# Kernel tuning notes

Measured on AMD Instinct MI355X. Metric: run time of the kernel, lower is better.

Reference implementation:

```python
import jax, jax.numpy as jnp
import numpy as np

N_NODES = 100000
N_EDGES = 1600000
D_IN = 128
D_HID = 128
D_OUT = 1
N_GRAPHS = 64


def setup_inputs() -> dict:
    key = jax.random.key(0)
    ks = jax.random.split(key, 8)
    x = jax.random.normal(ks[0], (N_NODES, D_IN), dtype=jnp.float32)
    edge_index = jax.random.randint(ks[1], (2, N_EDGES), 0, N_NODES, dtype=jnp.int64)
    batch = jnp.sort(jax.random.randint(ks[2], (N_NODES,), 0, N_GRAPHS, dtype=jnp.int64))
    s1 = 1.0 / np.sqrt(D_IN)
    s2 = 1.0 / np.sqrt(D_HID)
    W1 = jax.random.normal(ks[3], (D_IN, D_HID), dtype=jnp.float32) * s1
    b1 = jnp.zeros((D_HID,), dtype=jnp.float32)
    W2 = jax.random.normal(ks[4], (D_HID, D_HID), dtype=jnp.float32) * s2
    b2 = jnp.zeros((D_HID,), dtype=jnp.float32)
    Wf = jax.random.normal(ks[5], (D_HID, D_OUT), dtype=jnp.float32) * s2
    bf = jnp.zeros((D_OUT,), dtype=jnp.float32)
    return {"x": x, "edge_index": edge_index, "batch": batch,
            "W1": W1, "b1": b1, "W2": W2, "b2": b2, "Wf": Wf, "bf": bf,
            "num_graphs": N_GRAPHS}


def reference(x, edge_index, batch, W1, b1, W2, b2, Wf, bf, num_graphs):
    n = x.shape[0]
    # GCNConv default: add self-loops, symmetric deg^{-1/2} normalization
    loop = jnp.arange(n, dtype=edge_index.dtype)
    src = jnp.concatenate([edge_index[0], loop])  # [E+N]
    dst = jnp.concatenate([edge_index[1], loop])
    deg = jax.ops.segment_sum(jnp.ones(src.shape, x.dtype), dst, num_segments=n)
    dinv = jnp.where(deg > 0, jax.lax.rsqrt(jnp.maximum(deg, 1.0)), 0.0)
    norm = dinv[src] * dinv[dst]  # [E+N]

    def gcn_conv(h, W, b):
        h = h @ W  # [N, d_out] linear first (GCNConv fuses lin before propagate)
        msg = h[src] * norm[:, None]  # gather + scale
        return jax.ops.segment_sum(msg, dst, num_segments=n) + b  # scatter-add

    h = jax.nn.relu(gcn_conv(x, W1, b1))
    h = jax.nn.relu(gcn_conv(h, W2, b2))

    # global_mean_pool over batch assignment
    gsum = jax.ops.segment_sum(h, batch, num_segments=num_graphs)
    cnt = jax.ops.segment_sum(jnp.ones((n,), x.dtype), batch, num_segments=num_graphs)
    pooled = gsum / jnp.maximum(cnt, 1.0)[:, None]  # [G, d_hid]

    return (pooled @ Wf + bf).squeeze(-1)  # [G]
```

## Files before the change

### kernel.cpp

```cpp
#include <hip/hip_runtime.h>
#include <hip/hip_bf16.h>
#include <math.h>


#define DFEAT 128
#define SCAN_NB 256
#define SCAN_TPB 256
#define FILL_CHUNKS 256

typedef unsigned int uint32;
typedef __attribute__((ext_vector_type(8))) short bf16x8;
typedef __attribute__((ext_vector_type(4))) float f32x4;

__device__ __forceinline__ uint32 f2bf_rne(float f) {
    uint32 x = __float_as_uint(f);
    return (x + 0x7fffu + ((x >> 16) & 1u)) >> 16;
}
__device__ __forceinline__ uint32 packbf2(float lo, float hi) {
    return f2bf_rne(lo) | (f2bf_rne(hi) << 16);
}

__global__ void k_zero2(int* __restrict__ a, int* __restrict__ b, int n) {
    int i = blockIdx.x * blockDim.x + threadIdx.x;
    if (i < n) { a[i] = 0; b[i] = 0; }
}

__global__ void k_zero_f(float* __restrict__ p, int n) {
    int i = blockIdx.x * blockDim.x + threadIdx.x;
    if (i < n) p[i] = 0.f;
}

__global__ void k_degcount(const int* __restrict__ dst, int* __restrict__ degcnt, int E) {
    int e = blockIdx.x * blockDim.x + threadIdx.x;
    if (e < E) atomicAdd(&degcnt[dst[e]], 1);
}

__global__ __launch_bounds__(256) void k_wt(const float* __restrict__ W,
                                            unsigned short* __restrict__ Wt) {
    int idx = blockIdx.x * 256 + threadIdx.x;
    if (idx < 128 * 128) {
        int n = idx >> 7, k = idx & 127;
        Wt[idx] = (unsigned short)f2bf_rne(W[(k << 7) + n]);
    }
}

__global__ __launch_bounds__(SCAN_TPB) void k_partsum(const int* __restrict__ deg,
                                                      int* __restrict__ bsum,
                                                      int N, int chunk) {
    int b = blockIdx.x, tid = threadIdx.x;
    int beg = b * chunk, end = min(N, beg + chunk);
    int s = 0;
    for (int i = beg + tid; i < end; i += SCAN_TPB) s += deg[i];
    __shared__ int lds[SCAN_TPB];
    lds[tid] = s;
    __syncthreads();
    for (int off = SCAN_TPB / 2; off > 0; off >>= 1) {
        if (tid < off) lds[tid] += lds[tid + off];
        __syncthreads();
    }
    if (tid == 0) bsum[b] = lds[0];
}

__global__ __launch_bounds__(SCAN_NB) void k_scanb(int* __restrict__ bsum) {
    __shared__ int lds[SCAN_NB];
    int tid = threadIdx.x;
    int v = bsum[tid];
    lds[tid] = v;
    __syncthreads();
    for (int off = 1; off < SCAN_NB; off <<= 1) {
        int t = (tid >= off) ? lds[tid - off] : 0;
        __syncthreads();
        lds[tid] += t;
        __syncthreads();
    }
    bsum[tid] = lds[tid] - v;
}

__global__ __launch_bounds__(SCAN_TPB) void k_writeptr(const int* __restrict__ deg,
                                                       const int* __restrict__ bbase,
                                                       int* __restrict__ rowptr,
                                                       float* __restrict__ dinv,
                                                       int N, int chunk) {
    int b = blockIdx.x, tid = threadIdx.x;
    int beg = b * chunk, end = min(N, beg + chunk);
    int per = (chunk + SCAN_TPB - 1) / SCAN_TPB;
    int tbeg = beg + tid * per;
    int tend = min(end, tbeg + per);
    int s = 0;
    for (int i = tbeg; i < tend; ++i) s += deg[i];
    __shared__ int lds[SCAN_TPB];
    lds[tid] = s;
    __syncthreads();
    for (int off = 1; off < SCAN_TPB; off <<= 1) {
        int t = (tid >= off) ? lds[tid - off] : 0;
        __syncthreads();
        lds[tid] += t;
        __syncthreads();
    }
    int run = bbase[b] + ((tid == 0) ? 0 : lds[tid - 1]);
    for (int i = tbeg; i < tend; ++i) {
        int d = deg[i];
        rowptr[i] = run;
        dinv[i] = rsqrtf((float)(d + 1));
        run += d;
    }
    if (tend == N && tbeg < tend) rowptr[N] = run;
}

__global__ __launch_bounds__(256) void k_fill(const int* __restrict__ src,
                                              const int* __restrict__ dst,
                                              const int* __restrict__ rowptr,
                                              int* __restrict__ fill,
                                              int* __restrict__ col, int E) {
    int r = blockIdx.x & 7;
    int chunk = blockIdx.x >> 3;
    int per = (E + FILL_CHUNKS - 1) / FILL_CHUNKS;
    int beg = chunk * per;
    int end = min(E, beg + per);
    for (int e = beg + threadIdx.x; e < end; e += 256) {
        int d = dst[e];
        if (((d >> 9) & 7) == r) {
            int pos = rowptr[d] + atomicAdd(&fill[d], 1);
            col[pos] = src[e];
        }
    }
}

__global__ __launch_bounds__(256, 3) void k_linear_mfma(const float* __restrict__ H,
                                                        const uint32* __restrict__ Wt,
                                                        uint32* __restrict__ C,
                                                        int N, int ntiles) {
    __shared__ uint32 WtS[128 * 64];
    __shared__ uint32 inS[64 * 64];
    int tid = threadIdx.x;
    int lane = tid & 63;
    int wv = tid >> 6;
    int g = lane >> 4;
    int r = lane & 15;
    int swz = (r & 7) << 4;
    {
        const uint4* srcp = (const uint4*)Wt;
#pragma unroll
        for (int i = 0; i < 8; ++i) {
            int c = tid + i * 256;
            int n = c >> 4, off = c & 15;
            int b = (n * 256 + off * 16) ^ ((n & 7) << 4);
            *(uint4*)((char*)WtS + b) = srcp[c];
        }
    }
    for (int t = blockIdx.x; t < ntiles; t += gridDim.x) {
        int rbase = t << 6;
        __syncthreads();
        {
            const float4* H4 = (const float4*)(H + (size_t)rbase * DFEAT);
            int limrow = N - rbase;
#pragma unroll
            for (int i = 0; i < 4; ++i) {
                int c = tid + i * 256;
                int m = c >> 4, off = c & 15;
                uint4 w2 = make_uint4(0u, 0u, 0u, 0u);
                if (m < limrow) {
                    float4 f0 = H4[m * 32 + off * 2];
                    float4 f1 = H4[m * 32 + off * 2 + 1];
                    w2.x = packbf2(f0.x, f0.y); w2.y = packbf2(f0.z, f0.w);
                    w2.z = packbf2(f1.x, f1.y); w2.w = packbf2(f1.z, f1.w);
                }
                int b = (m * 256 + off * 16) ^ ((m & 7) << 4);
                *(uint4*)((char*)inS + b) = w2;
            }
        }
        __syncthreads();
        f32x4 acc[8];
#pragma unroll
        for (int nt = 0; nt < 8; ++nt) acc[nt] = (f32x4){0.f, 0.f, 0.f, 0.f};
        int mrow = wv * 16 + r;
        const char* inB = (const char*)inS + mrow * 256;
#pragma unroll
        for (int kk = 0; kk < 4; ++kk) {
            int koff = (kk * 64 + g * 16) ^ swz;
            bf16x8 bfrag = *(const bf16x8*)(inB + koff);
#pragma unroll
            for (int nt = 0; nt < 8; ++nt) {
                bf16x8 afrag = *(const bf16x8*)((const char*)WtS + (nt * 16 + r) * 256 + koff);
                acc[nt] = __builtin_amdgcn_mfma_f32_16x16x32_bf16(afrag, bfrag, acc[nt], 0, 0, 0);
            }
        }
        int m = rbase + mrow;
        if (m < N) {
            uint2* Crow = (uint2*)(C + (size_t)m * 64);
#pragma unroll
            for (int nt = 0; nt < 8; ++nt) {
                uint2 u;
                u.x = packbf2(acc[nt].x, acc[nt].y);
                u.y = packbf2(acc[nt].z, acc[nt].w);
                Crow[nt * 4 + g] = u;
            }
        }
    }
}

__global__ __launch_bounds__(256) void k_agg(const uint32* __restrict__ Tb,
                                             float2* __restrict__ Hout,
                                             const int* __restrict__ col,
                                             const int* __restrict__ rowptr,
                                             const float* __restrict__ dinv,
                                             const float* __restrict__ bias, int N) {
    int lane = threadIdx.x & 63;
    int node = blockIdx.x * 4 + (threadIdx.x >> 6);
    if (node >= N) return;
    float2 b = ((const float2*)bias)[lane];
    float di = dinv[node];
    uint32 us = Tb[(size_t)node * 64 + lane];
    float ws = di * di;
    float2 acc;
    acc.x = __uint_as_float(us << 16) * ws;
    acc.y = __uint_as_float(us & 0xffff0000u) * ws;
    int beg = rowptr[node], end = rowptr[node + 1];
    int j = beg;
    for (; j + 3 < end; j += 4) {
        int s0 = col[j + 0];
        int s1 = col[j + 1];
        int s2 = col[j + 2];
        int s3 = col[j + 3];
        float w0 = dinv[s0] * di;
        float w1 = dinv[s1] * di;
        float w2 = dinv[s2] * di;
        float w3 = dinv[s3] * di;
        uint32 u0 = Tb[(size_t)s0 * 64 + lane];
        uint32 u1 = Tb[(size_t)s1 * 64 + lane];
        uint32 u2 = Tb[(size_t)s2 * 64 + lane];
        uint32 u3 = Tb[(size_t)s3 * 64 + lane];
        acc.x += w0 * __uint_as_float(u0 << 16);
        acc.y += w0 * __uint_as_float(u0 & 0xffff0000u);
        acc.x += w1 * __uint_as_float(u1 << 16);
        acc.y += w1 * __uint_as_float(u1 & 0xffff0000u);
        acc.x += w2 * __uint_as_float(u2 << 16);
        acc.y += w2 * __uint_as_float(u2 & 0xffff0000u);
        acc.x += w3 * __uint_as_float(u3 << 16);
        acc.y += w3 * __uint_as_float(u3 & 0xffff0000u);
    }
    for (; j < end; ++j) {
        int s = col[j];
        float w = dinv[s] * di;
        uint32 u = Tb[(size_t)s * 64 + lane];
        acc.x += w * __uint_as_float(u << 16);
        acc.y += w * __uint_as_float(u & 0xffff0000u);
    }
    acc.x = fmaxf(acc.x + b.x, 0.f);
    acc.y = fmaxf(acc.y + b.y, 0.f);
    Hout[(size_t)node * 64 + lane] = acc;
}

__global__ __launch_bounds__(256) void k_pool_sum(const float2* __restrict__ Hn,
                                                  const int* __restrict__ batch,
                                                  float* __restrict__ gsum,
                                                  int N, int waves_total) {
    int w = blockIdx.x * 4 + (threadIdx.x >> 6);
    int lane = threadIdx.x & 63;
    int per = (N + waves_total - 1) / waves_total;
    int n0 = w * per;
    int n1 = min(N, n0 + per);
    if (n0 >= n1) return;
    int gcur = batch[n0];
    float2 acc = make_float2(0.f, 0.f);
    for (int i = n0; i < n1; ++i) {
        int g = batch[i];
        if (g != gcur) {
            atomicAdd(&gsum[gcur * DFEAT + lane * 2 + 0], acc.x);
            atomicAdd(&gsum[gcur * DFEAT + lane * 2 + 1], acc.y);
            acc = make_float2(0.f, 0.f);
            gcur = g;
        }
        float2 v = Hn[(size_t)i * 64 + lane];
        acc.x += v.x;
        acc.y += v.y;
    }
    atomicAdd(&gsum[gcur * DFEAT + lane * 2 + 0], acc.x);
    atomicAdd(&gsum[gcur * DFEAT + lane * 2 + 1], acc.y);
}

__global__ __launch_bounds__(128) void k_head(const float* __restrict__ gsum,
                                              const int* __restrict__ batch,
                                              const float* __restrict__ Wf,
                                              const float* __restrict__ bf,
                                              float* __restrict__ out, int N) {
    int g = blockIdx.x;
    int tid = threadIdx.x;
    int l = 0, h = N;
    while (l < h) { int m = (l + h) >> 1; if (batch[m] < g) l = m + 1; else h = m; }
    int lo = l;
    h = N;
    while (l < h) { int m = (l + h) >> 1; if (batch[m] < g + 1) l = m + 1; else h = m; }
    int hi = l;
    float cnt = (float)((hi - lo) > 0 ? (hi - lo) : 1);
    float val = (gsum[g * DFEAT + tid] / cnt) * Wf[tid];
    for (int off = 32; off >= 1; off >>= 1) val += __shfl_down(val, off, 64);
    __shared__ float ws2[2];
    if ((tid & 63) == 0) ws2[tid >> 6] = val;
    __syncthreads();
    if (tid == 0) out[g] = ws2[0] + ws2[1] + bf[0];
}

extern "C" void kernel_launch(void* const* d_in, const int* in_sizes, int n_in,
                              void* d_out, int out_size, void* d_ws, size_t ws_size,
                              hipStream_t stream) {
    const float* x    = (const float*)d_in[0];
    const int*   ei   = (const int*)d_in[1];
    const int*   batch= (const int*)d_in[2];
    const float* W1   = (const float*)d_in[3];
    const float* b1   = (const float*)d_in[4];
    const float* W2   = (const float*)d_in[5];
    const float* b2   = (const float*)d_in[6];
    const float* Wf   = (const float*)d_in[7];
    const float* bf   = (const float*)d_in[8];

    int N = in_sizes[0] / DFEAT;
    int E = in_sizes[1] / 2;
    int G = out_size;

    const int* src = ei;
    const int* dst = ei + E;

    char* wsb = (char*)d_ws;
    size_t off = 0;
    auto walloc = [&](size_t bytes) {
        void* p = wsb + off;
        off = (off + bytes + 255) & ~(size_t)255;
        return p;
    };
    uint32* A     = (uint32*)walloc((size_t)N * 64 * sizeof(uint32));
    float* B      = (float*)walloc((size_t)N * DFEAT * sizeof(float));
    float* dinv   = (float*)walloc((size_t)N * sizeof(float));
    int*   rowptr = (int*)  walloc((size_t)(N + 1) * sizeof(int));
    int*   col    = (int*)  walloc((size_t)E * sizeof(int));
    int*   degcnt = (int*)  walloc((size_t)N * sizeof(int));
    int*   fill   = (int*)  walloc((size_t)N * sizeof(int));
    float* gsum   = (float*)walloc((size_t)G * DFEAT * sizeof(float));
    int*   bsum   = (int*)  walloc((size_t)SCAN_NB * sizeof(int));
    unsigned short* Wt1 = (unsigned short*)walloc(128 * 128 * sizeof(unsigned short));
    unsigned short* Wt2 = (unsigned short*)walloc(128 * 128 * sizeof(unsigned short));
    (void)ws_size; (void)n_in;

    int gN = (N + 255) / 256;
    int gE = (E + 255) / 256;
    int chunk = (N + SCAN_NB - 1) / SCAN_NB;
    int ntiles = (N + 63) >> 6;

    k_zero2<<<gN, 256, 0, stream>>>(degcnt, fill, N);
    k_zero_f<<<(G * DFEAT + 255) / 256, 256, 0, stream>>>(gsum, G * DFEAT);
    k_wt<<<64, 256, 0, stream>>>(W1, Wt1);
    k_wt<<<64, 256, 0, stream>>>(W2, Wt2);
    k_degcount<<<gE, 256, 0, stream>>>(dst, degcnt, E);
    k_partsum<<<SCAN_NB, SCAN_TPB, 0, stream>>>(degcnt, bsum, N, chunk);
    k_scanb<<<1, SCAN_NB, 0, stream>>>(bsum);
    k_writeptr<<<SCAN_NB, SCAN_TPB, 0, stream>>>(degcnt, bsum, rowptr, dinv, N, chunk);
    k_fill<<<FILL_CHUNKS * 8, 256, 0, stream>>>(src, dst, rowptr, fill, col, E);

    k_linear_mfma<<<768, 256, 0, stream>>>(x, (const uint32*)Wt1, A, N, ntiles);
    k_agg<<<(N + 3) / 4, 256, 0, stream>>>(A, (float2*)B, col, rowptr, dinv, b1, N);
    k_linear_mfma<<<768, 256, 0, stream>>>(B, (const uint32*)Wt2, A, N, ntiles);
    k_agg<<<(N + 3) / 4, 256, 0, stream>>>(A, (float2*)B, col, rowptr, dinv, b2, N);

    const int POOL_BLOCKS = 1024;
    k_pool_sum<<<POOL_BLOCKS, 256, 0, stream>>>((const float2*)B, batch, gsum, N, POOL_BLOCKS * 4);
    k_head<<<G, 128, 0, stream>>>(gsum, batch, Wf, bf, (float*)d_out, N);
}
```

Measured before the change: 369.3 us.

## Split each wavefront across two neighbors in GCN aggregation with 8-byte gathers

The aggregation kernel now has each half-wave process a different neighbor, with lanes loading 4 bf16 values (uint2) instead of 2. The two halves are combined by a cross-lane shuffle and written as float4 by the lower half. This doubles the number of neighbor rows in flight per wave and widens the loads, to hide gather latency. The CSR fill kernel is also unrolled 4x so that several dst/src loads are outstanding before the atomics. The cost is a shuffle reduction, half the lanes idle during the store, and extra padded work for nodes with an odd degree.

```diff
diff --git a/kernel.cpp b/kernel.cpp
--- a/kernel.cpp
+++ b/kernel.cpp
@@ -19,6 +19,8 @@
 __device__ __forceinline__ uint32 packbf2(float lo, float hi) {
     return f2bf_rne(lo) | (f2bf_rne(hi) << 16);
 }
+__device__ __forceinline__ float bflo(uint32 u) { return __uint_as_float(u << 16); }
+__device__ __forceinline__ float bfhi(uint32 u) { return __uint_as_float(u & 0xffff0000u); }
 
 __global__ void k_zero2(int* __restrict__ a, int* __restrict__ b, int n) {
     int i = blockIdx.x * blockDim.x + threadIdx.x;
@@ -117,7 +119,16 @@
     int per = (E + FILL_CHUNKS - 1) / FILL_CHUNKS;
     int beg = chunk * per;
     int end = min(E, beg + per);
-    for (int e = beg + threadIdx.x; e < end; e += 256) {
+    int e = beg + threadIdx.x;
+    for (; e + 768 < end; e += 1024) {
+        int d0 = dst[e +   0], d1 = dst[e + 256], d2 = dst[e + 512], d3 = dst[e + 768];
+        int s0 = src[e +   0], s1 = src[e + 256], s2 = src[e + 512], s3 = src[e + 768];
+        if (((d0 >> 9) & 7) == r) { int p = rowptr[d0] + atomicAdd(&fill[d0], 1); col[p] = s0; }
+        if (((d1 >> 9) & 7) == r) { int p = rowptr[d1] + atomicAdd(&fill[d1], 1); col[p] = s1; }
+        if (((d2 >> 9) & 7) == r) { int p = rowptr[d2] + atomicAdd(&fill[d2], 1); col[p] = s2; }
+        if (((d3 >> 9) & 7) == r) { int p = rowptr[d3] + atomicAdd(&fill[d3], 1); col[p] = s3; }
+    }
+    for (; e < end; e += 256) {
         int d = dst[e];
         if (((d >> 9) & 7) == r) {
             int pos = rowptr[d] + atomicAdd(&fill[d], 1);
@@ -199,56 +210,61 @@
     }
 }
 
-__global__ __launch_bounds__(256) void k_agg(const uint32* __restrict__ Tb,
-                                             float2* __restrict__ Hout,
+__global__ __launch_bounds__(256) void k_agg(const uint2* __restrict__ T4,
+                                             float4* __restrict__ Hout,
                                              const int* __restrict__ col,
                                              const int* __restrict__ rowptr,
                                              const float* __restrict__ dinv,
                                              const float* __restrict__ bias, int N) {
     int lane = threadIdx.x & 63;
+    int half = lane >> 5;
+    int q = lane & 31;
     int node = blockIdx.x * 4 + (threadIdx.x >> 6);
     if (node >= N) return;
-    float2 b = ((const float2*)bias)[lane];
     float di = dinv[node];
-    uint32 us = Tb[(size_t)node * 64 + lane];
-    float ws = di * di;
-    float2 acc;
-    acc.x = __uint_as_float(us << 16) * ws;
-    acc.y = __uint_as_float(us & 0xffff0000u) * ws;
+    float4 acc;
+    {
+        uint2 u = T4[(size_t)node * 32 + q];
+        float ws = (half == 0) ? di * di : 0.f;
+        acc.x = ws * bflo(u.x); acc.y = ws * bfhi(u.x);
+        acc.z = ws * bflo(u.y); acc.w = ws * bfhi(u.y);
+    }
     int beg = rowptr[node], end = rowptr[node + 1];
     int j = beg;
     for (; j + 3 < end; j += 4) {
-        int s0 = col[j + 0];
-        int s1 = col[j + 1];
-        int s2 = col[j + 2];
-        int s3 = col[j + 3];
-        float w0 = dinv[s0] * di;
-        float w1 = dinv[s1] * di;
-        float w2 = dinv[s2] * di;
-        float w3 = dinv[s3] * di;
-        uint32 u0 = Tb[(size_t)s0 * 64 + lane];
-        uint32 u1 = Tb[(size_t)s1 * 64 + lane];
-        uint32 u2 = Tb[(size_t)s2 * 64 + lane];
-        uint32 u3 = Tb[(size_t)s3 * 64 + lane];
-        acc.x += w0 * __uint_as_float(u0 << 16);
-        acc.y += w0 * __uint_as_float(u0 & 0xffff0000u);
-        acc.x += w1 * __uint_as_float(u1 << 16);
-        acc.y += w1 * __uint_as_float(u1 & 0xffff0000u);
-        acc.x += w2 * __uint_as_float(u2 << 16);
-        acc.y += w2 * __uint_as_float(u2 & 0xffff0000u);
-        acc.x += w3 * __uint_as_float(u3 << 16);
-        acc.y += w3 * __uint_as_float(u3 & 0xffff0000u);
-    }
-    for (; j < end; ++j) {
-        int s = col[j];
-        float w = dinv[s] * di;
-        uint32 u = Tb[(size_t)s * 64 + lane];
-        acc.x += w * __uint_as_float(u << 16);
-        acc.y += w * __uint_as_float(u & 0xffff0000u);
-    }
-    acc.x = fmaxf(acc.x + b.x, 0.f);
-    acc.y = fmaxf(acc.y + b.y, 0.f);
-    Hout[(size_t)node * 64 + lane] = acc;
+        int sa = col[j + half];
+        int sb = col[j + 2 + half];
+        float wa = dinv[sa] * di;
+        float wb = dinv[sb] * di;
+        uint2 ua = T4[(size_t)sa * 32 + q];
+        uint2 ub = T4[(size_t)sb * 32 + q];
+        acc.x += wa * bflo(ua.x); acc.y += wa * bfhi(ua.x);
+        acc.z += wa * bflo(ua.y); acc.w += wa * bfhi(ua.y);
+        acc.x += wb * bflo(ub.x); acc.y += wb * bfhi(ub.x);
+        acc.z += wb * bflo(ub.y); acc.w += wb * bfhi(ub.y);
+    }
+    for (; j < end; j += 2) {
+        int jj = j + half;
+        bool valid = jj < end;
+        int s = valid ? col[jj] : node;
+        float w = valid ? dinv[s] * di : 0.f;
+        uint2 u = T4[(size_t)s * 32 + q];
+        acc.x += w * bflo(u.x); acc.y += w * bfhi(u.x);
+        acc.z += w * bflo(u.y); acc.w += w * bfhi(u.y);
+    }
+    acc.x += __shfl_xor(acc.x, 32, 64);
+    acc.y += __shfl_xor(acc.y, 32, 64);
+    acc.z += __shfl_xor(acc.z, 32, 64);
+    acc.w += __shfl_xor(acc.w, 32, 64);
+    if (half == 0) {
+        float4 b4 = ((const float4*)bias)[q];
+        float4 o;
+        o.x = fmaxf(acc.x + b4.x, 0.f);
+        o.y = fmaxf(acc.y + b4.y, 0.f);
+        o.z = fmaxf(acc.z + b4.z, 0.f);
+        o.w = fmaxf(acc.w + b4.w, 0.f);
+        Hout[(size_t)node * 32 + q] = o;
+    }
 }
 
 __global__ __launch_bounds__(256) void k_pool_sum(const float2* __restrict__ Hn,
@@ -357,9 +373,9 @@
     k_fill<<<FILL_CHUNKS * 8, 256, 0, stream>>>(src, dst, rowptr, fill, col, E);
 
     k_linear_mfma<<<768, 256, 0, stream>>>(x, (const uint32*)Wt1, A, N, ntiles);
-    k_agg<<<(N + 3) / 4, 256, 0, stream>>>(A, (float2*)B, col, rowptr, dinv, b1, N);
+    k_agg<<<(N + 3) / 4, 256, 0, stream>>>((const uint2*)A, (float4*)B, col, rowptr, dinv, b1, N);
     k_linear_mfma<<<768, 256, 0, stream>>>(B, (const uint32*)Wt2, A, N, ntiles);
-    k_agg<<<(N + 3) / 4, 256, 0, stream>>>(A, (float2*)B, col, rowptr, dinv, b2, N);
+    k_agg<<<(N + 3) / 4, 256, 0, stream>>>((const uint2*)A, (float4*)B, col, rowptr, dinv, b2, N);
 
     const int POOL_BLOCKS = 1024;
     k_pool_sum<<<POOL_BLOCKS, 256, 0, stream>>>((const float2*)B, batch, gsum, N, POOL_BLOCKS * 4);
```

After: 383.3 us. +3.8%, slower.
